# Kernel tuning notes

Hardware: AMD Instinct MI355X
Metric: run time of the kernel (lower is better)

Reference implementation:

```python
import jax, jax.numpy as jnp
import numpy as np

K = 8                   # num_RQS_bins
MIN_BW = 1e-6; MIN_BH = 1e-6; MIN_D = 1e-6
TAIL = 12.0             # tail_bound for 'linear' tails
# binary masks for num_inputs=4: kept (conditioning) dims and transformed dims per layer
MASK_IDX = [(0, 2), (1, 3), (0, 1), (2, 3)]
INV_IDX = [(1, 3), (0, 2), (2, 3), (0, 1)]


def _rqs_forward(x, uw, uh, ud):
    """Unconstrained rational-quadratic spline, forward (direct) pass.
    x: [B,F]; uw,uh: [B,F,K]; ud: [B,F,K-1]. Returns (y, logabsdet) each [B,F]."""
    const = float(np.log(np.exp(1.0 - MIN_D) - 1.0))
    ud = jnp.pad(ud, ((0, 0), (0, 0), (1, 1)), constant_values=const)  # [B,F,K+1]
    inside = (x >= -TAIL) & (x <= TAIL)
    xc = jnp.clip(x, -TAIL, TAIL)

    widths = MIN_BW + (1.0 - MIN_BW * K) * jax.nn.softmax(uw, -1)
    cumw = jnp.pad(jnp.cumsum(widths, -1), ((0, 0), (0, 0), (1, 0)))
    cumw = 2.0 * TAIL * cumw - TAIL
    cumw = cumw.at[..., 0].set(-TAIL).at[..., -1].set(TAIL)
    widths = cumw[..., 1:] - cumw[..., :-1]

    heights = MIN_BH + (1.0 - MIN_BH * K) * jax.nn.softmax(uh, -1)
    cumh = jnp.pad(jnp.cumsum(heights, -1), ((0, 0), (0, 0), (1, 0)))
    cumh = 2.0 * TAIL * cumh - TAIL
    cumh = cumh.at[..., 0].set(-TAIL).at[..., -1].set(TAIL)
    heights = cumh[..., 1:] - cumh[..., :-1]

    derivs = MIN_D + jax.nn.softplus(ud)  # [B,F,K+1]

    # searchsorted over bin edges (forward mode uses cumwidths)
    idx = jnp.clip(jnp.sum((xc[..., None] >= cumw).astype(jnp.int32), -1) - 1, 0, K - 1)
    g = lambda t: jnp.take_along_axis(t, idx[..., None], axis=-1)[..., 0]
    in_cw, in_w = g(cumw), g(widths)
    in_ch, in_h = g(cumh), g(heights)
    delta = in_h / in_w
    d_k, d_k1 = g(derivs), g(derivs[..., 1:])

    theta = (xc - in_cw) / in_w
    tomt = theta * (1.0 - theta)
    num = in_h * (delta * theta ** 2 + d_k * tomt)
    den = delta + (d_k + d_k1 - 2.0 * delta) * tomt
    y = in_ch + num / den
    dnum = delta ** 2 * (d_k1 * theta ** 2 + 2.0 * delta * tomt + d_k * (1.0 - theta) ** 2)
    lad = jnp.log(dnum) - 2.0 * jnp.log(den)

    return jnp.where(inside, y, x), jnp.where(inside, lad, 0.0)


def setup_inputs() -> dict:
    key = jax.random.key(0)
    ks = jax.random.split(key, 5)
    B, H = 262144, 128
    OM = 3 * K - 1  # 23 params per transformed dim
    inputs = jax.random.normal(ks[0], (B, 4), jnp.float32)
    cond_inputs = jax.random.uniform(ks[1], (B, 1), jnp.float32)
    W1 = jax.random.normal(ks[2], (4, H, 3), jnp.float32) / np.sqrt(3.0)
    b1 = jnp.zeros((4, H), jnp.float32)
    W2 = jax.random.normal(ks[3], (4, H, H), jnp.float32) / np.sqrt(float(H))
    b2 = jnp.zeros((4, H), jnp.float32)
    W3 = jax.random.normal(ks[4], (4, 2 * OM, H), jnp.float32) / np.sqrt(float(H))
    b3 = jnp.zeros((4, 2 * OM), jnp.float32)
    return {"inputs": inputs, "cond_inputs": cond_inputs,
            "W1": W1, "b1": b1, "W2": W2, "b2": b2, "W3": W3, "b3": b3}


def reference(inputs, cond_inputs, W1, b1, W2, b2, W3, b3):
    B = inputs.shape[0]
    x = inputs
    logdets = jnp.zeros((B, 1), dtype=inputs.dtype)
    for l in range(4):  # fixed small number of coupling layers
        midx = list(MASK_IDX[l]); iidx = list(INV_IDX[l])
        m_in = jnp.concatenate([x[:, midx], cond_inputs], -1)  # [B,3]
        h = jax.nn.relu(m_in @ W1[l].T + b1[l])
        h = jax.nn.relu(h @ W2[l].T + b2[l])
        params = h @ W3[l].T + b3[l]  # [B, F*(3K-1)]
        F = len(iidx)
        tp = jnp.swapaxes(params.reshape(B, 3 * K - 1, F), 1, 2)  # [B,F,3K-1]
        y, lad = _rqs_forward(x[:, iidx], tp[..., :K], tp[..., K:2 * K], tp[..., 2 * K:])
        x = x.at[:, iidx].set(y)
        logdets = logdets + jnp.sum(lad, -1, keepdims=True)
    return x, logdets
```

## Files before the change

kernel.cpp:

```cpp
#include <hip/hip_runtime.h>

#define TAILB 12.0f
#define INV2048 4.8828125e-4f

typedef _Float16 half8 __attribute__((ext_vector_type(8)));
typedef _Float16 half4 __attribute__((ext_vector_type(4)));
typedef __fp16 fp16x2 __attribute__((ext_vector_type(2)));
typedef __attribute__((ext_vector_type(4))) float f32x4;

#define MFMAH __builtin_amdgcn_mfma_f32_16x16x32_f16

__device__ __forceinline__ float softplus_f(float z) {
    return (z > 15.f) ? z : __logf(1.f + __expf(z));
}

__device__ __forceinline__ void split2h(float v, _Float16& o0, _Float16& o1) {
    _Float16 h0 = (_Float16)v;
    float r1 = v - (float)h0;
    o0 = h0;
    o1 = (_Float16)(r1 * 2048.0f);
}

__device__ __forceinline__ void split4_pk(const float* v, half4& p0, half4& p1) {
    fp16x2 lo = __builtin_amdgcn_cvt_pkrtz(v[0], v[1]);
    fp16x2 hi = __builtin_amdgcn_cvt_pkrtz(v[2], v[3]);
    float r0 = (v[0] - (float)lo.x) * 2048.f;
    float r1 = (v[1] - (float)lo.y) * 2048.f;
    float r2 = (v[2] - (float)hi.x) * 2048.f;
    float r3 = (v[3] - (float)hi.y) * 2048.f;
    fp16x2 rlo = __builtin_amdgcn_cvt_pkrtz(r0, r1);
    fp16x2 rhi = __builtin_amdgcn_cvt_pkrtz(r2, r3);
    p0 = (half4){(_Float16)lo.x, (_Float16)lo.y, (_Float16)hi.x, (_Float16)hi.y};
    p1 = (half4){(_Float16)rlo.x, (_Float16)rlo.y, (_Float16)rhi.x, (_Float16)rhi.y};
}

__global__ __launch_bounds__(256)
void prep_v15(const float* __restrict__ W1, const float* __restrict__ b1,
              const float* __restrict__ W2, const float* __restrict__ W3,
              _Float16* __restrict__ W2F, _Float16* __restrict__ W3F,
              float4* __restrict__ w1p)
{
    int id = blockIdx.x * 256 + threadIdx.x;
    if (id < 65536) {
        int j = id & 7, ln = (id >> 3) & 63, tile = id >> 9;
        int cs = tile & 3, t = (tile >> 2) & 1, wv = (tile >> 3) & 3, l = tile >> 5;
        int n = 32 * wv + 16 * t + (ln & 15);
        int k = 32 * cs + 8 * (ln >> 4) + j;
        _Float16 a, b;
        split2h(W2[l * 16384 + n * 128 + k], a, b);
        W2F[(tile * 2 + 0) * 512 + ln * 8 + j] = a;
        W2F[(tile * 2 + 1) * 512 + ln * 8 + j] = b;
    } else if (id < 90112) {
        int t2 = id - 65536;
        int j = t2 & 7, ln = (t2 >> 3) & 63, tile3 = t2 >> 9;
        int cs = tile3 & 3, q = tile3 >> 2;
        int wv = q % 3, l = q / 3;
        int p = 16 * wv + (ln & 15);
        int n = 32 * cs + 8 * (ln >> 4) + j;
        float v = (p < 46) ? W3[l * 5888 + p * 128 + n] : 0.f;
        _Float16 a, b;
        split2h(v, a, b);
        W3F[(tile3 * 2 + 0) * 512 + ln * 8 + j] = a;
        W3F[(tile3 * 2 + 1) * 512 + ln * 8 + j] = b;
    } else if (id < 90624) {
        int t = id - 90112;
        int l = t >> 7, k = t & 127;
        float4 v;
        v.x = W1[l * 384 + k * 3 + 0];
        v.y = W1[l * 384 + k * 3 + 1];
        v.z = W1[l * 384 + k * 3 + 2];
        v.w = b1[l * 128 + k];
        w1p[t] = v;
    }
}

__global__ __launch_bounds__(256, 3)
void rqs_v15(const float* __restrict__ inp, const float* __restrict__ cond,
             const _Float16* __restrict__ W2F, const _Float16* __restrict__ W3F,
             const float4* __restrict__ w1p,
             const float* __restrict__ b2, const float* __restrict__ b3,
             float* __restrict__ out, int B)
{
    __shared__ __align__(16) _Float16 planes[2][2][32][128];
    __shared__ float xbuf[32][5];

    char* plw = (char*)&planes[0][0][0][0];
    const char* pl = plw;
    float* ladb = (float*)(plw + 6656);

    const int tid  = threadIdx.x;
    const int base = blockIdx.x * 32;
    const int wv   = tid >> 6;
    const int ln   = tid & 63;
    const int sm   = ln & 15;
    const int qd   = ln >> 4;
    const int s1   = tid & 31;
    const int kh   = tid >> 5;

    int rdaddr[2][4];
    #pragma unroll
    for (int st = 0; st < 2; ++st)
        #pragma unroll
        for (int cs = 0; cs < 4; ++cs)
            rdaddr[st][cs] = (16 * st + sm) * 256 + (((4 * cs + qd) ^ sm) << 4);
    int wra[2];
    #pragma unroll
    for (int gi = 0; gi < 2; ++gi)
        wra[gi] = s1 * 256 + (((2 * kh + gi) ^ (s1 & 15)) << 4);
    int ewa[2][2];
    #pragma unroll
    for (int t = 0; t < 2; ++t)
        #pragma unroll
        for (int st = 0; st < 2; ++st) {
            int g = 4 * wv + 2 * t + (qd >> 1);
            ewa[t][st] = 16384 + (16 * st + sm) * 256 + ((g ^ sm) << 4) + ((qd & 1) << 3);
        }
    int pwa[2];
    #pragma unroll
    for (int st = 0; st < 2; ++st)
        pwa[st] = (16 * st + sm) * 208 + (16 * wv + 4 * qd) * 4;

    if (tid < 32) {
        float4 xi = reinterpret_cast<const float4*>(inp)[base + tid];
        xbuf[tid][0] = xi.x; xbuf[tid][1] = xi.y;
        xbuf[tid][2] = xi.z; xbuf[tid][3] = xi.w;
        xbuf[tid][4] = cond[base + tid];
    }
    float ladreg = 0.f;
    __syncthreads();

    #pragma unroll 1
    for (int l = 0; l < 4; ++l) {
        int mi0, mi1, ii0, ii1;
        switch (l) {
            case 0:  mi0 = 0; mi1 = 2; ii0 = 1; ii1 = 3; break;
            case 1:  mi0 = 1; mi1 = 3; ii0 = 0; ii1 = 2; break;
            case 2:  mi0 = 0; mi1 = 1; ii0 = 2; ii1 = 3; break;
            default: mi0 = 2; mi1 = 3; ii0 = 0; ii1 = 1; break;
        }

        {
            float m0 = xbuf[s1][mi0], m1 = xbuf[s1][mi1], cc = xbuf[s1][4];
            const float4* w1l = w1p + l * 128;
            #pragma unroll
            for (int gi = 0; gi < 2; ++gi) {
                int kb = (2 * kh + gi) * 8;
                float v[8];
                #pragma unroll
                for (int r = 0; r < 8; ++r) {
                    float4 w4 = w1l[kb + r];
                    v[r] = fmaxf(fmaf(w4.x, m0, fmaf(w4.y, m1, fmaf(w4.z, cc, w4.w))), 0.f);
                }
                half4 a0, a1, b0h, b1h;
                split4_pk(v, a0, a1);
                split4_pk(v + 4, b0h, b1h);
                half8 p0 = {a0.x, a0.y, a0.z, a0.w, b0h.x, b0h.y, b0h.z, b0h.w};
                half8 p1 = {a1.x, a1.y, a1.z, a1.w, b1h.x, b1h.y, b1h.z, b1h.w};
                char* wp = plw + wra[gi];
                *(half8*)(wp)        = p0;
                *(half8*)(wp + 8192) = p1;
            }
        }
        __syncthreads();

        f32x4 accA[2][2], accB[2][2];
        {
            int nb = __builtin_amdgcn_readfirstlane(l * 128 + 32 * wv);
            #pragma unroll
            for (int t = 0; t < 2; ++t) {
                float4 bias = *(const float4*)(b2 + nb + 16 * t + 4 * qd);
                #pragma unroll
                for (int st = 0; st < 2; ++st) {
                    accA[t][st] = (f32x4){bias.x, bias.y, bias.z, bias.w};
                    accB[t][st] = (f32x4){0.f, 0.f, 0.f, 0.f};
                }
            }
            const half8* W2F8 = (const half8*)W2F;
            int tb = (l * 4 + wv) * 2;
            #pragma unroll
            for (int cs = 0; cs < 4; ++cs) {
                half8 A00 = W2F8[(((tb + 0) * 4 + cs) * 2 + 0) * 64 + ln];
                half8 A01 = W2F8[(((tb + 0) * 4 + cs) * 2 + 1) * 64 + ln];
                half8 A10 = W2F8[(((tb + 1) * 4 + cs) * 2 + 0) * 64 + ln];
                half8 A11 = W2F8[(((tb + 1) * 4 + cs) * 2 + 1) * 64 + ln];
                #pragma unroll
                for (int st = 0; st < 2; ++st) {
                    half8 b0 = *(const half8*)(pl + rdaddr[st][cs]);
                    half8 b1 = *(const half8*)(pl + rdaddr[st][cs] + 8192);
                    accA[0][st] = MFMAH(A00, b0, accA[0][st], 0, 0, 0);
                    accB[0][st] = MFMAH(A00, b1, accB[0][st], 0, 0, 0);
                    accB[0][st] = MFMAH(A01, b0, accB[0][st], 0, 0, 0);
                    accA[1][st] = MFMAH(A10, b0, accA[1][st], 0, 0, 0);
                    accB[1][st] = MFMAH(A10, b1, accB[1][st], 0, 0, 0);
                    accB[1][st] = MFMAH(A11, b0, accB[1][st], 0, 0, 0);
                }
            }
        }

        {
            #pragma unroll
            for (int t = 0; t < 2; ++t) {
                #pragma unroll
                for (int st = 0; st < 2; ++st) {
                    float v[4];
                    #pragma unroll
                    for (int r = 0; r < 4; ++r)
                        v[r] = fmaxf(fmaf(INV2048, accB[t][st][r], accA[t][st][r]), 0.f);
                    half4 p0, p1;
                    split4_pk(v, p0, p1);
                    char* wp = plw + ewa[t][st];
                    *(half4*)(wp)        = p0;
                    *(half4*)(wp + 8192) = p1;
                }
            }
        }
        __syncthreads();

        f32x4 acc3A[2], acc3B[2];
        #pragma unroll
        for (int st = 0; st < 2; ++st) {
            acc3A[st] = (f32x4){0.f, 0.f, 0.f, 0.f};
            acc3B[st] = (f32x4){0.f, 0.f, 0.f, 0.f};
        }
        if (wv < 3) {
            const half8* W3F8 = (const half8*)W3F;
            int qb = (l * 3 + wv) * 4;
            #pragma unroll
            for (int cs = 0; cs < 4; ++cs) {
                half8 A0 = W3F8[((qb + cs) * 2 + 0) * 64 + ln];
                half8 A1 = W3F8[((qb + cs) * 2 + 1) * 64 + ln];
                #pragma unroll
                for (int st = 0; st < 2; ++st) {
                    half8 b0 = *(const half8*)(pl + 16384 + rdaddr[st][cs]);
                    half8 b1 = *(const half8*)(pl + 16384 + rdaddr[st][cs] + 8192);
                    acc3A[st] = MFMAH(A0, b0, acc3A[st], 0, 0, 0);
                    acc3B[st] = MFMAH(A0, b1, acc3B[st], 0, 0, 0);
                    acc3B[st] = MFMAH(A1, b0, acc3B[st], 0, 0, 0);
                }
            }
            #pragma unroll
            for (int st = 0; st < 2; ++st) {
                float4 pv;
                pv.x = fmaf(INV2048, acc3B[st][0], acc3A[st][0]);
                pv.y = fmaf(INV2048, acc3B[st][1], acc3A[st][1]);
                pv.z = fmaf(INV2048, acc3B[st][2], acc3A[st][2]);
                pv.w = fmaf(INV2048, acc3B[st][3], acc3A[st][3]);
                *(float4*)(plw + pwa[st]) = pv;
            }
        }
        __syncthreads();

        if (tid < 64) {
            int f = tid >> 5, s = tid & 31;
            const float* b3l = b3 + l * 46;
            const float4* prow = (const float4*)(pl + s * 208);
            float pr[23];
            #pragma unroll
            for (int i = 0; i < 12; ++i) {
                float4 q = prow[i];
                pr[2 * i] = (f ? q.y : q.x) + b3l[4 * i + f];
                if (2 * i + 1 < 23)
                    pr[2 * i + 1] = (f ? q.w : q.z) + b3l[4 * i + 2 + f];
            }

            float xin = xbuf[s][f == 0 ? ii0 : ii1];

            float d[9];
            d[0] = 1.f; d[8] = 1.f;
            #pragma unroll
            for (int k = 1; k < 8; ++k) d[k] = 1e-6f + softplus_f(pr[16 + k - 1]);

            bool inside = (xin >= -TAILB) && (xin <= TAILB);
            float xc = fminf(fmaxf(xin, -TAILB), TAILB);

            float mw = pr[0], mh = pr[8];
            #pragma unroll
            for (int k = 1; k < 8; ++k) { mw = fmaxf(mw, pr[k]); mh = fmaxf(mh, pr[8 + k]); }
            float ew[8], eh[8], swm = 0.f, shm = 0.f;
            #pragma unroll
            for (int k = 0; k < 8; ++k) {
                ew[k] = __expf(pr[k] - mw);     swm += ew[k];
                eh[k] = __expf(pr[8 + k] - mh); shm += eh[k];
            }
            const float c1 = 1.f - 8e-6f;
            float isw = __fdividef(c1, swm), ish = __fdividef(c1, shm);

            float cum_w = 0.f, cum_h = 0.f;
            float cwk = -TAILB, chk = -TAILB;
            float s_cw = -TAILB, s_w = 2.f * TAILB, s_ch = -TAILB, s_h = 2.f * TAILB;
            float s_d0 = 1.f, s_d1 = d[1];
            #pragma unroll
            for (int k = 0; k < 8; ++k) {
                cum_w += fmaf(ew[k], isw, 1e-6f);
                cum_h += fmaf(eh[k], ish, 1e-6f);
                float cwn = (k == 7) ? TAILB : fmaf(2.f * TAILB, cum_w, -TAILB);
                float chn = (k == 7) ? TAILB : fmaf(2.f * TAILB, cum_h, -TAILB);
                bool ge = (xc >= cwk);
                s_cw = ge ? cwk : s_cw;  s_w = ge ? (cwn - cwk) : s_w;
                s_ch = ge ? chk : s_ch;  s_h = ge ? (chn - chk) : s_h;
                s_d0 = ge ? d[k] : s_d0; s_d1 = ge ? d[k + 1] : s_d1;
                cwk = cwn; chk = chn;
            }

            float rw    = __fdividef(1.f, s_w);
            float th    = (xc - s_cw) * rw;
            float delta = s_h * rw;
            float omt   = 1.f - th;
            float tomt  = th * omt;
            float num   = s_h * fmaf(delta, th * th, s_d0 * tomt);
            float den   = fmaf(s_d0 + s_d1 - 2.f * delta, tomt, delta);
            float y     = s_ch + __fdividef(num, den);
            float dnum  = delta * delta * (s_d1 * th * th + 2.f * delta * tomt + s_d0 * omt * omt);
            float lad   = __logf(dnum) - 2.f * __logf(den);

            xbuf[s][f == 0 ? ii0 : ii1] = inside ? y : xin;
            ladreg += inside ? lad : 0.f;
        }
        __syncthreads();
    }

    if (tid < 64) ladb[tid] = ladreg;
    __syncthreads();
    if (tid < 32) {
        float4 xo;
        xo.x = xbuf[tid][0]; xo.y = xbuf[tid][1];
        xo.z = xbuf[tid][2]; xo.w = xbuf[tid][3];
        reinterpret_cast<float4*>(out)[base + tid] = xo;
        out[(size_t)B * 4 + base + tid] = ladb[tid] + ladb[tid + 32];
    }
}

extern "C" void kernel_launch(void* const* d_in, const int* in_sizes, int n_in,
                              void* d_out, int out_size, void* d_ws, size_t ws_size,
                              hipStream_t stream) {
    const float* inp  = (const float*)d_in[0];
    const float* cond = (const float*)d_in[1];
    const float* W1   = (const float*)d_in[2];
    const float* b1   = (const float*)d_in[3];
    const float* W2   = (const float*)d_in[4];
    const float* b2   = (const float*)d_in[5];
    const float* W3   = (const float*)d_in[6];
    const float* b3   = (const float*)d_in[7];
    float* out = (float*)d_out;
    int B = in_sizes[0] / 4;

    char* ws = (char*)d_ws;
    _Float16* W2F = (_Float16*)(ws);
    _Float16* W3F = (_Float16*)(ws + 262144);
    float4*   w1p = (float4*)(ws + 360448);

    hipLaunchKernelGGL(prep_v15, dim3(354), dim3(256), 0, stream,
                       W1, b1, W2, W3, W2F, W3F, w1p);
    hipLaunchKernelGGL(rqs_v15, dim3(B / 32), dim3(256), 0, stream,
                       inp, cond, W2F, W3F, w1p, b2, b3, out, B);
}
```

Baseline: 277.4 us.

## Restructure RQS flow kernel to a single wave per 32-sample block

```diff
diff --git a/kernel.cpp b/kernel.cpp
--- a/kernel.cpp
+++ b/kernel.cpp
@@ -35,7 +35,7 @@
 }
 
 __global__ __launch_bounds__(256)
-void prep_v15(const float* __restrict__ W1, const float* __restrict__ b1,
+void prep_v16(const float* __restrict__ W1, const float* __restrict__ b1,
               const float* __restrict__ W2, const float* __restrict__ W3,
               _Float16* __restrict__ W2F, _Float16* __restrict__ W3F,
               float4* __restrict__ w1p)
@@ -74,57 +74,41 @@
     }
 }
 
-__global__ __launch_bounds__(256, 3)
-void rqs_v15(const float* __restrict__ inp, const float* __restrict__ cond,
+__global__ __launch_bounds__(64, 3)
+void rqs_v16(const float* __restrict__ inp, const float* __restrict__ cond,
              const _Float16* __restrict__ W2F, const _Float16* __restrict__ W3F,
              const float4* __restrict__ w1p,
              const float* __restrict__ b2, const float* __restrict__ b3,
              float* __restrict__ out, int B)
 {
-    __shared__ __align__(16) _Float16 planes[2][2][32][128];
+    __shared__ __align__(16) _Float16 h2planes[2][32][128];
     __shared__ float xbuf[32][5];
 
-    char* plw = (char*)&planes[0][0][0][0];
+    char* plw = (char*)&h2planes[0][0][0];
     const char* pl = plw;
+    float* pbuf = (float*)plw;
     float* ladb = (float*)(plw + 6656);
 
-    const int tid  = threadIdx.x;
-    const int base = blockIdx.x * 32;
-    const int wv   = tid >> 6;
-    const int ln   = tid & 63;
+    const int ln   = threadIdx.x;
     const int sm   = ln & 15;
     const int qd   = ln >> 4;
-    const int s1   = tid & 31;
-    const int kh   = tid >> 5;
-
-    int rdaddr[2][4];
+    const int base = blockIdx.x * 32;
+
+    int srow[2], ksr[2], rda[2][4];
     #pragma unroll
-    for (int st = 0; st < 2; ++st)
+    for (int g2 = 0; g2 < 2; ++g2) {
+        srow[g2] = sm + 16 * g2;
+        ksr[g2]  = (srow[g2] & 15) << 1;
         #pragma unroll
         for (int cs = 0; cs < 4; ++cs)
-            rdaddr[st][cs] = (16 * st + sm) * 256 + (((4 * cs + qd) ^ sm) << 4);
-    int wra[2];
-    #pragma unroll
-    for (int gi = 0; gi < 2; ++gi)
-        wra[gi] = s1 * 256 + (((2 * kh + gi) ^ (s1 & 15)) << 4);
-    int ewa[2][2];
-    #pragma unroll
-    for (int t = 0; t < 2; ++t)
-        #pragma unroll
-        for (int st = 0; st < 2; ++st) {
-            int g = 4 * wv + 2 * t + (qd >> 1);
-            ewa[t][st] = 16384 + (16 * st + sm) * 256 + ((g ^ sm) << 4) + ((qd & 1) << 3);
-        }
-    int pwa[2];
-    #pragma unroll
-    for (int st = 0; st < 2; ++st)
-        pwa[st] = (16 * st + sm) * 208 + (16 * wv + 4 * qd) * 4;
-
-    if (tid < 32) {
-        float4 xi = reinterpret_cast<const float4*>(inp)[base + tid];
-        xbuf[tid][0] = xi.x; xbuf[tid][1] = xi.y;
-        xbuf[tid][2] = xi.z; xbuf[tid][3] = xi.w;
-        xbuf[tid][4] = cond[base + tid];
+            rda[g2][cs] = srow[g2] * 256 + (((8 * cs + 2 * qd) ^ ksr[g2]) << 3);
+    }
+
+    if (ln < 32) {
+        float4 xi = reinterpret_cast<const float4*>(inp)[base + ln];
+        xbuf[ln][0] = xi.x; xbuf[ln][1] = xi.y;
+        xbuf[ln][2] = xi.z; xbuf[ln][3] = xi.w;
+        xbuf[ln][4] = cond[base + ln];
     }
     float ladreg = 0.f;
     __syncthreads();
@@ -139,121 +123,128 @@
             default: mi0 = 2; mi1 = 3; ii0 = 0; ii1 = 1; break;
         }
 
+        half8 h1f[2][4][2];
         {
-            float m0 = xbuf[s1][mi0], m1 = xbuf[s1][mi1], cc = xbuf[s1][4];
+            float m0[2], m1[2], cc[2];
+            #pragma unroll
+            for (int g2 = 0; g2 < 2; ++g2) {
+                m0[g2] = xbuf[srow[g2]][mi0];
+                m1[g2] = xbuf[srow[g2]][mi1];
+                cc[g2] = xbuf[srow[g2]][4];
+            }
             const float4* w1l = w1p + l * 128;
             #pragma unroll
-            for (int gi = 0; gi < 2; ++gi) {
-                int kb = (2 * kh + gi) * 8;
-                float v[8];
-                #pragma unroll
-                for (int r = 0; r < 8; ++r) {
-                    float4 w4 = w1l[kb + r];
-                    v[r] = fmaxf(fmaf(w4.x, m0, fmaf(w4.y, m1, fmaf(w4.z, cc, w4.w))), 0.f);
-                }
-                half4 a0, a1, b0h, b1h;
-                split4_pk(v, a0, a1);
-                split4_pk(v + 4, b0h, b1h);
-                half8 p0 = {a0.x, a0.y, a0.z, a0.w, b0h.x, b0h.y, b0h.z, b0h.w};
-                half8 p1 = {a1.x, a1.y, a1.z, a1.w, b1h.x, b1h.y, b1h.z, b1h.w};
-                char* wp = plw + wra[gi];
-                *(half8*)(wp)        = p0;
-                *(half8*)(wp + 8192) = p1;
-            }
-        }
-        __syncthreads();
-
-        f32x4 accA[2][2], accB[2][2];
+            for (int cs = 0; cs < 4; ++cs) {
+                float4 w4[8];
+                #pragma unroll
+                for (int j = 0; j < 8; ++j) w4[j] = w1l[32 * cs + 8 * qd + j];
+                #pragma unroll
+                for (int g2 = 0; g2 < 2; ++g2) {
+                    float v[8];
+                    #pragma unroll
+                    for (int j = 0; j < 8; ++j)
+                        v[j] = fmaxf(fmaf(w4[j].x, m0[g2],
+                                     fmaf(w4[j].y, m1[g2],
+                                     fmaf(w4[j].z, cc[g2], w4[j].w))), 0.f);
+                    half4 a0, a1, b0, b1;
+                    split4_pk(v, a0, a1);
+                    split4_pk(v + 4, b0, b1);
+                    h1f[g2][cs][0] = (half8){a0.x, a0.y, a0.z, a0.w, b0.x, b0.y, b0.z, b0.w};
+                    h1f[g2][cs][1] = (half8){a1.x, a1.y, a1.z, a1.w, b1.x, b1.y, b1.z, b1.w};
+                }
+            }
+        }
+
         {
-            int nb = __builtin_amdgcn_readfirstlane(l * 128 + 32 * wv);
-            #pragma unroll
-            for (int t = 0; t < 2; ++t) {
-                float4 bias = *(const float4*)(b2 + nb + 16 * t + 4 * qd);
-                #pragma unroll
-                for (int st = 0; st < 2; ++st) {
-                    accA[t][st] = (f32x4){bias.x, bias.y, bias.z, bias.w};
-                    accB[t][st] = (f32x4){0.f, 0.f, 0.f, 0.f};
-                }
-            }
             const half8* W2F8 = (const half8*)W2F;
-            int tb = (l * 4 + wv) * 2;
-            #pragma unroll
-            for (int cs = 0; cs < 4; ++cs) {
-                half8 A00 = W2F8[(((tb + 0) * 4 + cs) * 2 + 0) * 64 + ln];
-                half8 A01 = W2F8[(((tb + 0) * 4 + cs) * 2 + 1) * 64 + ln];
-                half8 A10 = W2F8[(((tb + 1) * 4 + cs) * 2 + 0) * 64 + ln];
-                half8 A11 = W2F8[(((tb + 1) * 4 + cs) * 2 + 1) * 64 + ln];
-                #pragma unroll
-                for (int st = 0; st < 2; ++st) {
-                    half8 b0 = *(const half8*)(pl + rdaddr[st][cs]);
-                    half8 b1 = *(const half8*)(pl + rdaddr[st][cs] + 8192);
-                    accA[0][st] = MFMAH(A00, b0, accA[0][st], 0, 0, 0);
-                    accB[0][st] = MFMAH(A00, b1, accB[0][st], 0, 0, 0);
-                    accB[0][st] = MFMAH(A01, b0, accB[0][st], 0, 0, 0);
-                    accA[1][st] = MFMAH(A10, b0, accA[1][st], 0, 0, 0);
-                    accB[1][st] = MFMAH(A10, b1, accB[1][st], 0, 0, 0);
-                    accB[1][st] = MFMAH(A11, b0, accB[1][st], 0, 0, 0);
-                }
-            }
-        }
-
-        {
-            #pragma unroll
-            for (int t = 0; t < 2; ++t) {
-                #pragma unroll
-                for (int st = 0; st < 2; ++st) {
+            #pragma unroll 1
+            for (int nt = 0; nt < 8; ++nt) {
+                half8 A0[4], A1[4];
+                #pragma unroll
+                for (int cs = 0; cs < 4; ++cs) {
+                    int tile = ((l * 4 + (nt >> 1)) * 2 + (nt & 1)) * 4 + cs;
+                    A0[cs] = W2F8[(tile * 2 + 0) * 64 + ln];
+                    A1[cs] = W2F8[(tile * 2 + 1) * 64 + ln];
+                }
+                float4 bv = *(const float4*)(b2 + l * 128 + 16 * nt + 4 * qd);
+                f32x4 aA[2], aB[2];
+                #pragma unroll
+                for (int g2 = 0; g2 < 2; ++g2) {
+                    aA[g2] = (f32x4){bv.x, bv.y, bv.z, bv.w};
+                    aB[g2] = (f32x4){0.f, 0.f, 0.f, 0.f};
+                }
+                #pragma unroll
+                for (int cs = 0; cs < 4; ++cs) {
+                    #pragma unroll
+                    for (int g2 = 0; g2 < 2; ++g2) {
+                        aA[g2] = MFMAH(A0[cs], h1f[g2][cs][0], aA[g2], 0, 0, 0);
+                        aB[g2] = MFMAH(A0[cs], h1f[g2][cs][1], aB[g2], 0, 0, 0);
+                        aB[g2] = MFMAH(A1[cs], h1f[g2][cs][0], aB[g2], 0, 0, 0);
+                    }
+                }
+                #pragma unroll
+                for (int g2 = 0; g2 < 2; ++g2) {
                     float v[4];
                     #pragma unroll
                     for (int r = 0; r < 4; ++r)
-                        v[r] = fmaxf(fmaf(INV2048, accB[t][st][r], accA[t][st][r]), 0.f);
+                        v[r] = fmaxf(fmaf(INV2048, aB[g2][r], aA[g2][r]), 0.f);
                     half4 p0, p1;
                     split4_pk(v, p0, p1);
-                    char* wp = plw + ewa[t][st];
-                    *(half4*)(wp)        = p0;
-                    *(half4*)(wp + 8192) = p1;
+                    int wadr = srow[g2] * 256 + (((4 * nt + qd) ^ ksr[g2]) << 3);
+                    *(half4*)(plw + wadr)        = p0;
+                    *(half4*)(plw + 8192 + wadr) = p1;
                 }
             }
         }
         __syncthreads();
 
-        f32x4 acc3A[2], acc3B[2];
+        f32x4 pA[3][2], pB[3][2];
         #pragma unroll
-        for (int st = 0; st < 2; ++st) {
-            acc3A[st] = (f32x4){0.f, 0.f, 0.f, 0.f};
-            acc3B[st] = (f32x4){0.f, 0.f, 0.f, 0.f};
-        }
-        if (wv < 3) {
+        for (int pt = 0; pt < 3; ++pt)
+            #pragma unroll
+            for (int g2 = 0; g2 < 2; ++g2) {
+                pA[pt][g2] = (f32x4){0.f, 0.f, 0.f, 0.f};
+                pB[pt][g2] = (f32x4){0.f, 0.f, 0.f, 0.f};
+            }
+        {
             const half8* W3F8 = (const half8*)W3F;
-            int qb = (l * 3 + wv) * 4;
-            #pragma unroll
-            for (int cs = 0; cs < 4; ++cs) {
-                half8 A0 = W3F8[((qb + cs) * 2 + 0) * 64 + ln];
-                half8 A1 = W3F8[((qb + cs) * 2 + 1) * 64 + ln];
-                #pragma unroll
-                for (int st = 0; st < 2; ++st) {
-                    half8 b0 = *(const half8*)(pl + 16384 + rdaddr[st][cs]);
-                    half8 b1 = *(const half8*)(pl + 16384 + rdaddr[st][cs] + 8192);
-                    acc3A[st] = MFMAH(A0, b0, acc3A[st], 0, 0, 0);
-                    acc3B[st] = MFMAH(A0, b1, acc3B[st], 0, 0, 0);
-                    acc3B[st] = MFMAH(A1, b0, acc3B[st], 0, 0, 0);
-                }
-            }
-            #pragma unroll
-            for (int st = 0; st < 2; ++st) {
+            #pragma unroll 1
+            for (int pt = 0; pt < 3; ++pt) {
+                int qb = (l * 3 + pt) * 4;
+                #pragma unroll
+                for (int cs = 0; cs < 4; ++cs) {
+                    half8 A0 = W3F8[((qb + cs) * 2 + 0) * 64 + ln];
+                    half8 A1 = W3F8[((qb + cs) * 2 + 1) * 64 + ln];
+                    #pragma unroll
+                    for (int g2 = 0; g2 < 2; ++g2) {
+                        half8 b0 = *(const half8*)(pl + rda[g2][cs]);
+                        half8 b1 = *(const half8*)(pl + 8192 + rda[g2][cs]);
+                        pA[pt][g2] = MFMAH(A0, b0, pA[pt][g2], 0, 0, 0);
+                        pB[pt][g2] = MFMAH(A0, b1, pB[pt][g2], 0, 0, 0);
+                        pB[pt][g2] = MFMAH(A1, b0, pB[pt][g2], 0, 0, 0);
+                    }
+                }
+            }
+        }
+        __syncthreads();
+
+        #pragma unroll
+        for (int pt = 0; pt < 3; ++pt)
+            #pragma unroll
+            for (int g2 = 0; g2 < 2; ++g2) {
                 float4 pv;
-                pv.x = fmaf(INV2048, acc3B[st][0], acc3A[st][0]);
-                pv.y = fmaf(INV2048, acc3B[st][1], acc3A[st][1]);
-                pv.z = fmaf(INV2048, acc3B[st][2], acc3A[st][2]);
-                pv.w = fmaf(INV2048, acc3B[st][3], acc3A[st][3]);
-                *(float4*)(plw + pwa[st]) = pv;
-            }
-        }
+                pv.x = fmaf(INV2048, pB[pt][g2][0], pA[pt][g2][0]);
+                pv.y = fmaf(INV2048, pB[pt][g2][1], pA[pt][g2][1]);
+                pv.z = fmaf(INV2048, pB[pt][g2][2], pA[pt][g2][2]);
+                pv.w = fmaf(INV2048, pB[pt][g2][3], pA[pt][g2][3]);
+                *(float4*)((char*)pbuf + srow[g2] * 208 + (16 * pt + 4 * qd) * 4) = pv;
+            }
         __syncthreads();
 
-        if (tid < 64) {
-            int f = tid >> 5, s = tid & 31;
+        {
+            int f = ln >> 5, s = ln & 31;
             const float* b3l = b3 + l * 46;
-            const float4* prow = (const float4*)(pl + s * 208);
+            const float4* prow = (const float4*)((const char*)pbuf + s * 208);
             float pr[23];
             #pragma unroll
             for (int i = 0; i < 12; ++i) {
@@ -319,14 +310,14 @@
         __syncthreads();
     }
 
-    if (tid < 64) ladb[tid] = ladreg;
+    ladb[ln] = ladreg;
     __syncthreads();
-    if (tid < 32) {
+    if (ln < 32) {
         float4 xo;
-        xo.x = xbuf[tid][0]; xo.y = xbuf[tid][1];
-        xo.z = xbuf[tid][2]; xo.w = xbuf[tid][3];
-        reinterpret_cast<float4*>(out)[base + tid] = xo;
-        out[(size_t)B * 4 + base + tid] = ladb[tid] + ladb[tid + 32];
+        xo.x = xbuf[ln][0]; xo.y = xbuf[ln][1];
+        xo.z = xbuf[ln][2]; xo.w = xbuf[ln][3];
+        reinterpret_cast<float4*>(out)[base + ln] = xo;
+        out[(size_t)B * 4 + base + ln] = ladb[ln] + ladb[ln + 32];
     }
 }
 
@@ -349,8 +340,8 @@
     _Float16* W3F = (_Float16*)(ws + 262144);
     float4*   w1p = (float4*)(ws + 360448);
 
-    hipLaunchKernelGGL(prep_v15, dim3(354), dim3(256), 0, stream,
+    hipLaunchKernelGGL(prep_v16, dim3(354), dim3(256), 0, stream,
                        W1, b1, W2, W3, W2F, W3F, w1p);
-    hipLaunchKernelGGL(rqs_v15, dim3(B / 32), dim3(256), 0, stream,
+    hipLaunchKernelGGL(rqs_v16, dim3(B / 32), dim3(64), 0, stream,
                        inp, cond, W2F, W3F, w1p, b2, b3, out, B);
 }
```

Result: slower. 335.6 us (+21.0%).
